# Kernel optimization log

Measured on AMD Instinct MI355X. Metric: run time of the kernel, lower is better.

Reference implementation:

```python
import jax, jax.numpy as jnp
import numpy as np

HEADS = 4
N_ROUNDS = 2
R_LSH = 1.0
PH, PW = 8, 8  # patch size


def _forward(x, Wq, Wk, Wv, Wo, alpha, beta, q_w, q_b, fmam_w, fmam_b, dw_w):
    b, c, H, W = x.shape
    nh, nw = H // PH, W // PW
    # b,c,H,W -> b,H,W,c -> (b*nh*nw, PH*PW, c) patch sequences
    xi = jnp.transpose(x, (0, 2, 3, 1))
    xp = xi.reshape(b, nh, PH, nw, PW, c).transpose(0, 1, 3, 2, 4, 5)
    xp = xp.reshape(b * nh * nw, PH * PW, c)
    B, N, _ = xp.shape

    q = xp @ Wq  # (B,N,3c)
    k = xp @ Wk
    v = xp @ Wv
    d = q.shape[-1] // HEADS

    def split_heads(t):
        # 'b t (h e) -> (b h) t e'
        return t.reshape(B, N, HEADS, -1).transpose(0, 2, 1, 3).reshape(B * HEADS, N, -1)

    qh, kh, vh = split_heads(q), split_heads(k), split_heads(v)
    xh = split_heads(xp)  # (bs, N, c/heads) used for hashing

    # XBOX+ asymmetric transform (no_grad in original)
    norms = jnp.linalg.norm(xh, axis=-1, keepdims=True)            # (bs,N,1)
    MX = jnp.max(norms, axis=-2, keepdims=True)                    # (bs,1,1)
    ext = jnp.sqrt(jnp.maximum(MX ** 2 - norms ** 2, 0.0))
    Xs = jnp.concatenate([xh, ext, jnp.zeros_like(ext)], axis=-1)  # (bs,N,e+2)

    # SALSH projections -> bucket order via argsort
    proj = (Xs @ alpha + beta) / R_LSH                             # (bs,N,R)
    pos = jax.lax.stop_gradient(jnp.argsort(jnp.transpose(proj, (2, 0, 1)), axis=-1))  # (R,bs,N)

    def gather(t):  # (bs,N,d) -> (R,bs,N,d) permuted per round
        return jnp.take_along_axis(jnp.broadcast_to(t, (N_ROUNDS,) + t.shape), pos[..., None], axis=2)

    sq, sk, sv = gather(qh), gather(kh), gather(vh)
    # block == whole 64-token patch, attention within permuted block
    inner = jnp.einsum('rbqd,rbkd->rbqk', sq, sk)                  # (R,bs,N,N)
    lse = jax.scipy.special.logsumexp(inner, axis=-1, keepdims=True)
    dots = jnp.exp(inner - lse)
    bo = jnp.einsum('rbqk,rbkd->rbqd', dots, sv)                   # (R,bs,N,d)

    rev = jnp.argsort(pos, axis=-1)                                # inverse permutation
    o = jnp.take_along_axis(bo, rev[..., None], axis=2)            # scatter back
    logits = jnp.take_along_axis(lse[..., 0], rev, axis=2)         # (R,bs,N)
    probs = jnp.exp(logits - jax.scipy.special.logsumexp(logits, axis=0, keepdims=True))
    out = jnp.sum(o * probs[..., None], axis=0)                    # (bs,N,d)

    out = out.reshape(B, HEADS, N, d).transpose(0, 2, 1, 3).reshape(B, N, HEADS * d)
    out = out @ Wo                                                 # (B,N,c)
    F_spa = out.reshape(b, nh, nw, PH, PW, c).transpose(0, 1, 3, 2, 4, 5).reshape(b, H, W, c)
    spa = jnp.transpose(F_spa, (0, 3, 1, 2))                       # (b,c,H,W)

    # FMAM stand-in: global-context module producing (b,c,c) frequency context
    xf = x.reshape(b, c, H * W)
    keys = jax.nn.softmax(jnp.einsum('oc,bcn->bon', fmam_w, xf) + fmam_b[None, :, None], axis=-1)
    ctx = jnp.einsum('bcn,bon->bco', xf, keys)                     # (b,c,c)
    queries = jax.nn.softmax(jnp.einsum('oc,bcn->bon', q_w, xf) + q_b[None, :, None], axis=1)
    freq = jnp.einsum('bck,bcn->bkn', ctx, queries).reshape(b, c, H, W)

    # depthwise Conv3d kernel (2,1,1), no bias -> per-channel weighted sum
    return spa * dw_w[:, 0][None, :, None, None] + freq * dw_w[:, 1][None, :, None, None]


def setup_inputs() -> dict:
    key = jax.random.key(0)
    ks = jax.random.split(key, 12)
    b, c, H, W = 2, 64, 256, 256
    inner = 3 * c
    e = c // HEADS
    s = 0.02
    return {
        'x': jax.random.normal(ks[0], (b, c, H, W), jnp.float32),
        'Wq': jax.random.normal(ks[1], (c, inner), jnp.float32) * s,
        'Wk': jax.random.normal(ks[2], (c, inner), jnp.float32) * s,
        'Wv': jax.random.normal(ks[3], (c, inner), jnp.float32) * s,
        'Wo': jax.random.normal(ks[4], (inner, c), jnp.float32) * s,
        'alpha': jax.random.normal(ks[5], (e + 2, N_ROUNDS), jnp.float32),
        'beta': jax.random.uniform(ks[6], (1, N_ROUNDS), jnp.float32, 0.0, R_LSH),
        'q_w': jax.random.normal(ks[7], (c, c), jnp.float32) * s,
        'q_b': jnp.zeros((c,), jnp.float32),
        'fmam_w': jax.random.normal(ks[8], (c, c), jnp.float32) * s,
        'fmam_b': jnp.zeros((c,), jnp.float32),
        'dw_w': jax.random.normal(ks[9], (c, 2), jnp.float32) * 0.5,
    }


def reference(x, Wq, Wk, Wv, Wo, alpha, beta, q_w, q_b, fmam_w, fmam_b, dw_w):
    return _forward(x, Wq, Wk, Wv, Wo, alpha, beta, q_w, q_b, fmam_w, fmam_b, dw_w)
```

## Files before the change

### kernel.cpp

```cpp
#include <hip/hip_runtime.h>
#include <hip/hip_bf16.h>


typedef __attribute__((ext_vector_type(8))) short bf16x8;
typedef __attribute__((ext_vector_type(4))) float f32x4;
typedef __attribute__((ext_vector_type(4))) unsigned u32x4;

static __device__ __forceinline__ short f2bf(float f) {
  __hip_bfloat16 h = __float2bfloat16(f);
  return *reinterpret_cast<short*>(&h);
}
static __device__ __forceinline__ float bf2f(short s) {
  return __uint_as_float(((unsigned)(unsigned short)s) << 16);
}
static __device__ __forceinline__ unsigned pack2bf(float a, float b) {
  return (unsigned)(unsigned short)f2bf(a) | ((unsigned)(unsigned short)f2bf(b) << 16);
}
static __device__ __forceinline__ f32x4 MFMA(bf16x8 a, bf16x8 b, f32x4 c) {
  return __builtin_amdgcn_mfma_f32_16x16x32_bf16(a, b, c, 0, 0, 0);
}

#define LSWZ(row, bytecol) ((((row) << 7) + (bytecol)) ^ (((row) & 7) << 4))

static __device__ __forceinline__ bf16x8 repack(
    unsigned pl0, unsigned pl1, unsigned ph0, unsigned ph1,
    int srcA, int srcB, bool hi) {
  unsigned l0 = __shfl((int)pl0, srcA, 64), l1 = __shfl((int)pl1, srcA, 64);
  unsigned l2 = __shfl((int)pl0, srcB, 64), l3 = __shfl((int)pl1, srcB, 64);
  unsigned h0 = __shfl((int)ph0, srcA, 64), h1 = __shfl((int)ph1, srcA, 64);
  unsigned h2 = __shfl((int)ph0, srcB, 64), h3 = __shfl((int)ph1, srcB, 64);
  u32x4 v;
  v[0] = hi ? h0 : l0; v[1] = hi ? h1 : l1;
  v[2] = hi ? h2 : l2; v[3] = hi ? h3 : l3;
  return __builtin_bit_cast(bf16x8, v);
}
static __device__ __forceinline__ bf16x8 repack1(
    unsigned pl0, unsigned pl1, int srcA, int srcB, bool hi) {
  unsigned l0 = __shfl((int)pl0, srcA, 64), l1 = __shfl((int)pl1, srcA, 64);
  unsigned l2 = __shfl((int)pl0, srcB, 64), l3 = __shfl((int)pl1, srcB, 64);
  u32x4 v;
  v[0] = hi ? 0u : l0; v[1] = hi ? 0u : l1;
  v[2] = hi ? 0u : l2; v[3] = hi ? 0u : l3;
  return __builtin_bit_cast(bf16x8, v);
}

static __device__ __forceinline__ bf16x8 load_xfrag(const float* xg, int c0, int n) {
  bf16x8 r;
#pragma unroll
  for (int j = 0; j < 8; ++j) r[j] = f2bf(xg[((size_t)(c0 + j) << 16) + (size_t)n]);
  return r;
}

__global__ __launch_bounds__(256) void prep_w(
    const float* __restrict__ Wq, const float* __restrict__ Wk,
    const float* __restrict__ Wv, const float* __restrict__ Wo,
    const float* __restrict__ fw, const float* __restrict__ qw,
    short* __restrict__ Wt3, short* __restrict__ Wvb,
    short* __restrict__ WoT2, short* __restrict__ fwb, short* __restrict__ qwb)
{
  int i = blockIdx.x * 256 + threadIdx.x;
  if (i < 24576) {
    int m = i / 12288, rem = i % 12288;
    int r = rem >> 6, c = rem & 63;
    const float* W = m ? Wk : Wq;
    Wt3[i] = f2bf(W[c * 192 + r]);
  }
  if (i < 12288) {
    int h = i / 3072, rem = i % 3072;
    int j = rem & 7, ln = (rem >> 3) & 63, dcks = rem >> 9;
    int dc = dcks >> 1, ks = dcks & 1;
    int c = 32 * ks + 8 * (ln >> 4) + j;
    int col = 48 * h + 16 * dc + (ln & 15);
    Wvb[i] = f2bf(Wv[c * 192 + col]);
  }
  if (i < 12288) {
    int co = i / 192, dg = i % 192;
    WoT2[i] = f2bf(Wo[dg * 64 + co]);
  }
  if (i < 4096) { fwb[i] = f2bf(fw[i]); qwb[i] = f2bf(qw[i]); }
}

__global__ __launch_bounds__(256, 3) void attn_fused(
    const float* __restrict__ x, const short* __restrict__ Wt3,
    const short* __restrict__ Wvb, const short* __restrict__ WoT2,
    const short* __restrict__ qwb, const float* __restrict__ qbias,
    const short* __restrict__ ctxb16, const float* __restrict__ dw,
    float* __restrict__ out)
{
  __shared__ __align__(16) char ob_[25600];
  char* xb_ = ob_;

  const int tid = threadIdx.x, lane = tid & 63, w = tid >> 6;
  const int l15 = lane & 15, l4 = lane >> 4;
  const int srcA = l15 + 32 * (l4 & 1), srcB = srcA + 16;
  const bool hi = (l4 & 2) != 0;

  const int pid0 = blockIdx.x;
  const int pid = (pid0 & 7) * 256 + (pid0 >> 3);
  const int b = pid >> 10, prem = pid & 1023;
  const int y0 = (prem >> 5) << 3, x0 = (prem & 31) << 3;
  const float* xg = x + ((size_t)b << 22);

#pragma unroll
  for (int k = 0; k < 2; ++k) {
    int idx = tid + (k << 8);
    int t = idx & 63, c0 = (idx >> 6) << 3;
    const size_t pos = (size_t)((y0 + (t >> 3)) * 256 + x0 + (t & 7));
    bf16x8 v;
#pragma unroll
    for (int j = 0; j < 8; ++j) v[j] = f2bf(xg[((size_t)(c0 + j) << 16) + pos]);
    *(bf16x8*)(xb_ + LSWZ(t, c0 * 2)) = v;
  }
  __syncthreads();

  const int h = w;

  unsigned qpk[3][4][2], kpk[3][4][2];
#pragma unroll
  for (int m = 0; m < 2; ++m) {
    const short* WT = Wt3 + m * 12288 + (48 * h) * 64;
    bf16x8 a[3][2];
#pragma unroll
    for (int rp = 0; rp < 3; ++rp)
#pragma unroll
      for (int ks = 0; ks < 2; ++ks)
        a[rp][ks] = *(const bf16x8*)(WT + (16 * rp + l15) * 64 + 32 * ks + 8 * l4);
    __builtin_amdgcn_s_setprio(1);
#pragma unroll
    for (int cq = 0; cq < 4; ++cq) {
      bf16x8 b0 = *(const bf16x8*)(xb_ + LSWZ(16 * cq + l15, 16 * l4));
      bf16x8 b1 = *(const bf16x8*)(xb_ + LSWZ(16 * cq + l15, 64 + 16 * l4));
#pragma unroll
      for (int rp = 0; rp < 3; ++rp) {
        f32x4 acc = (f32x4)0.f;
        acc = MFMA(a[rp][0], b0, acc);
        acc = MFMA(a[rp][1], b1, acc);
        unsigned* dst = m ? kpk[rp][cq] : qpk[rp][cq];
        dst[0] = pack2bf(acc[0], acc[1]);
        dst[1] = pack2bf(acc[2], acc[3]);
      }
    }
    __builtin_amdgcn_s_setprio(0);
  }

  unsigned ppk[4][4][2];
  {
    bf16x8 Bq[4][2];
#pragma unroll
    for (int tt = 0; tt < 4; ++tt) {
      Bq[tt][0] = repack(qpk[0][tt][0], qpk[0][tt][1], qpk[1][tt][0], qpk[1][tt][1], srcA, srcB, hi);
      Bq[tt][1] = repack1(qpk[2][tt][0], qpk[2][tt][1], srcA, srcB, hi);
    }
    f32x4 st[4][4];
#pragma unroll
    for (int ur = 0; ur < 4; ++ur) {
      bf16x8 A0 = repack(kpk[0][ur][0], kpk[0][ur][1], kpk[1][ur][0], kpk[1][ur][1], srcA, srcB, hi);
      bf16x8 A1 = repack1(kpk[2][ur][0], kpk[2][ur][1], srcA, srcB, hi);
      __builtin_amdgcn_s_setprio(1);
#pragma unroll
      for (int tt = 0; tt < 4; ++tt) {
        f32x4 acc = (f32x4)0.f;
        acc = MFMA(A0, Bq[tt][0], acc);
        acc = MFMA(A1, Bq[tt][1], acc);
        st[ur][tt] = acc;
      }
      __builtin_amdgcn_s_setprio(0);
    }
#pragma unroll
    for (int tt = 0; tt < 4; ++tt) {
      float m = st[0][tt][0];
#pragma unroll
      for (int ur = 0; ur < 4; ++ur)
#pragma unroll
        for (int r = 0; r < 4; ++r) m = fmaxf(m, st[ur][tt][r]);
      m = fmaxf(m, __shfl_xor(m, 16, 64));
      m = fmaxf(m, __shfl_xor(m, 32, 64));
      float s = 0.f;
#pragma unroll
      for (int ur = 0; ur < 4; ++ur)
#pragma unroll
        for (int r = 0; r < 4; ++r) {
          float e = __expf(st[ur][tt][r] - m);
          st[ur][tt][r] = e; s += e;
        }
      s += __shfl_xor(s, 16, 64);
      s += __shfl_xor(s, 32, 64);
      const float inv = 1.f / s;
#pragma unroll
      for (int ur = 0; ur < 4; ++ur) {
        ppk[ur][tt][0] = pack2bf(st[ur][tt][0] * inv, st[ur][tt][1] * inv);
        ppk[ur][tt][1] = pack2bf(st[ur][tt][2] * inv, st[ur][tt][3] * inv);
      }
    }
  }

  unsigned vpk[4][3][2];
  {
    const short* Wvh = Wvb + h * 3072;
    bf16x8 bv[3][2];
#pragma unroll
    for (int dc = 0; dc < 3; ++dc)
#pragma unroll
      for (int ks = 0; ks < 2; ++ks)
        bv[dc][ks] = *(const bf16x8*)(Wvh + ((dc * 2 + ks) * 64 + lane) * 8);
    __builtin_amdgcn_s_setprio(1);
#pragma unroll
    for (int ur = 0; ur < 4; ++ur) {
      bf16x8 a0 = *(const bf16x8*)(xb_ + LSWZ(16 * ur + l15, 16 * l4));
      bf16x8 a1 = *(const bf16x8*)(xb_ + LSWZ(16 * ur + l15, 64 + 16 * l4));
#pragma unroll
      for (int dc = 0; dc < 3; ++dc) {
        f32x4 acc = (f32x4)0.f;
        acc = MFMA(a0, bv[dc][0], acc);
        acc = MFMA(a1, bv[dc][1], acc);
        vpk[ur][dc][0] = pack2bf(acc[0], acc[1]);
        vpk[ur][dc][1] = pack2bf(acc[2], acc[3]);
      }
    }
    __builtin_amdgcn_s_setprio(0);
  }

  unsigned pzpk[4][2];
  {
    bf16x8 xz0 = *(const bf16x8*)(xb_ + LSWZ(16 * w + l15, 16 * l4));
    bf16x8 xz1 = *(const bf16x8*)(xb_ + LSWZ(16 * w + l15, 64 + 16 * l4));
    f32x4 zt[4];
#pragma unroll
    for (int orr = 0; orr < 4; ++orr) {
      bf16x8 a0 = *(const bf16x8*)(qwb + (16 * orr + l15) * 64 + 8 * l4);
      bf16x8 a1 = *(const bf16x8*)(qwb + (16 * orr + l15) * 64 + 32 + 8 * l4);
      f32x4 acc;
#pragma unroll
      for (int r = 0; r < 4; ++r) acc[r] = qbias[16 * orr + 4 * l4 + r];
      acc = MFMA(a0, xz0, acc);
      acc = MFMA(a1, xz1, acc);
      zt[orr] = acc;
    }
    float m = zt[0][0];
#pragma unroll
    for (int orr = 0; orr < 4; ++orr)
#pragma unroll
      for (int r = 0; r < 4; ++r) m = fmaxf(m, zt[orr][r]);
    m = fmaxf(m, __shfl_xor(m, 16, 64));
    m = fmaxf(m, __shfl_xor(m, 32, 64));
    float s = 0.f;
#pragma unroll
    for (int orr = 0; orr < 4; ++orr)
#pragma unroll
      for (int r = 0; r < 4; ++r) { float e = __expf(zt[orr][r] - m); zt[orr][r] = e; s += e; }
    s += __shfl_xor(s, 16, 64);
    s += __shfl_xor(s, 32, 64);
    const float inv = 1.f / s;
#pragma unroll
    for (int orr = 0; orr < 4; ++orr) {
      pzpk[orr][0] = pack2bf(zt[orr][0] * inv, zt[orr][1] * inv);
      pzpk[orr][1] = pack2bf(zt[orr][2] * inv, zt[orr][3] * inv);
    }
  }
  __syncthreads();

  {
    bf16x8 Bp[4][2];
#pragma unroll
    for (int tt = 0; tt < 4; ++tt) {
      Bp[tt][0] = repack(ppk[0][tt][0], ppk[0][tt][1], ppk[1][tt][0], ppk[1][tt][1], srcA, srcB, hi);
      Bp[tt][1] = repack(ppk[2][tt][0], ppk[2][tt][1], ppk[3][tt][0], ppk[3][tt][1], srcA, srcB, hi);
    }
#pragma unroll
    for (int dr = 0; dr < 3; ++dr) {
      bf16x8 A0 = repack(vpk[0][dr][0], vpk[0][dr][1], vpk[1][dr][0], vpk[1][dr][1], srcA, srcB, hi);
      bf16x8 A1 = repack(vpk[2][dr][0], vpk[2][dr][1], vpk[3][dr][0], vpk[3][dr][1], srcA, srcB, hi);
      __builtin_amdgcn_s_setprio(1);
#pragma unroll
      for (int tt = 0; tt < 4; ++tt) {
        f32x4 acc = (f32x4)0.f;
        acc = MFMA(A0, Bp[tt][0], acc);
        acc = MFMA(A1, Bp[tt][1], acc);
        const int row = 16 * tt + l15;
        const int col = 48 * h + 16 * dr + 4 * l4;
        *(unsigned*)(ob_ + row * 400 + col * 2)     = pack2bf(acc[0], acc[1]);
        *(unsigned*)(ob_ + row * 400 + col * 2 + 4) = pack2bf(acc[2], acc[3]);
      }
      __builtin_amdgcn_s_setprio(0);
    }
  }
  __syncthreads();

  {
    f32x4 ot[4], ft[4];
#pragma unroll
    for (int kr = 0; kr < 4; ++kr) { ot[kr] = (f32x4)0.f; ft[kr] = (f32x4)0.f; }
    __builtin_amdgcn_s_setprio(1);
#pragma unroll
    for (int ks = 0; ks < 6; ++ks) {
      bf16x8 bo = *(const bf16x8*)(ob_ + (16 * w + l15) * 400 + 64 * ks + 16 * l4);
#pragma unroll
      for (int kr = 0; kr < 4; ++kr) {
        bf16x8 a = *(const bf16x8*)(WoT2 + (16 * kr + l15) * 192 + 32 * ks + 8 * l4);
        ot[kr] = MFMA(a, bo, ot[kr]);
      }
    }
    {
      bf16x8 Bz0 = repack(pzpk[0][0], pzpk[0][1], pzpk[1][0], pzpk[1][1], srcA, srcB, hi);
      bf16x8 Bz1 = repack(pzpk[2][0], pzpk[2][1], pzpk[3][0], pzpk[3][1], srcA, srcB, hi);
      const short* cb = ctxb16 + ((size_t)b << 12);
#pragma unroll
      for (int kr = 0; kr < 4; ++kr) {
        bf16x8 a0 = *(const bf16x8*)(cb + (16 * kr + l15) * 64 + 8 * l4);
        bf16x8 a1 = *(const bf16x8*)(cb + (16 * kr + l15) * 64 + 32 + 8 * l4);
        ft[kr] = MFMA(a0, Bz0, ft[kr]);
        ft[kr] = MFMA(a1, Bz1, ft[kr]);
      }
    }
    __builtin_amdgcn_s_setprio(0);
    const int t = 16 * w + l15;
    const size_t nbase = (size_t)((y0 + (t >> 3)) * 256 + x0 + (t & 7));
    float* og = out + ((size_t)b << 22);
#pragma unroll
    for (int kr = 0; kr < 4; ++kr)
#pragma unroll
      for (int r = 0; r < 4; ++r) {
        const int co = 16 * kr + 4 * l4 + r;
        og[((size_t)co << 16) + nbase] = ot[kr][r] * dw[2 * co] + ft[kr][r] * dw[2 * co + 1];
      }
  }
}

__global__ __launch_bounds__(256) void fmam_ctx1(
    const float* __restrict__ x, const short* __restrict__ fwb,
    const float* __restrict__ fb, float* __restrict__ ctxpart,
    float* __restrict__ epart)
{
  __shared__ short cred16[4][64 * 68];
  __shared__ float ered[4][64];
  const int tid = threadIdx.x, lane = tid & 63, w = tid >> 6;
  const int l15 = lane & 15, l4 = lane >> 4;
  const int srcA = l15 + 32 * (l4 & 1), srcB = srcA + 16;
  const bool hi = (l4 & 2) != 0;
  const int chunk = blockIdx.x, b = blockIdx.y;
  const float* xg = x + ((size_t)b << 22);
  const int n0 = (chunk << 8) + (w << 6);

  bf16x8 Bfw[4][2];
#pragma unroll
  for (int ct = 0; ct < 4; ++ct)
#pragma unroll
    for (int ks = 0; ks < 2; ++ks)
      Bfw[ct][ks] = *(const bf16x8*)(fwb + (16 * ct + l15) * 64 + 32 * ks + 8 * l4);
  float fbl[4];
#pragma unroll
  for (int ct = 0; ct < 4; ++ct) fbl[ct] = fb[16 * ct + l15];

  f32x4 acc[4][4];
#pragma unroll
  for (int i = 0; i < 4; ++i)
#pragma unroll
    for (int j = 0; j < 4; ++j) acc[i][j] = (f32x4)0.f;
  float esum[4] = {0.f, 0.f, 0.f, 0.f};

#pragma unroll
  for (int ns = 0; ns < 2; ++ns) {
    const int nb = n0 + 32 * ns;
    bf16x8 axT[2][2];
#pragma unroll
    for (int rt = 0; rt < 2; ++rt)
#pragma unroll
      for (int ks = 0; ks < 2; ++ks)
        axT[rt][ks] = load_xfrag(xg, 32 * ks + 8 * l4, nb + 16 * rt + l15);
    unsigned pl[4][2][2];
#pragma unroll
    for (int rt = 0; rt < 2; ++rt)
#pragma unroll
      for (int ct = 0; ct < 4; ++ct) {
        f32x4 yt = (f32x4)(fbl[ct]);
        yt = MFMA(axT[rt][0], Bfw[ct][0], yt);
        yt = MFMA(axT[rt][1], Bfw[ct][1], yt);
        float e0 = __expf(yt[0]), e1 = __expf(yt[1]);
        float e2 = __expf(yt[2]), e3 = __expf(yt[3]);
        esum[ct] += (e0 + e1) + (e2 + e3);
        pl[ct][rt][0] = pack2bf(e0, e1);
        pl[ct][rt][1] = pack2bf(e2, e3);
      }
    bf16x8 axc[4];
#pragma unroll
    for (int rt2 = 0; rt2 < 4; ++rt2) {
      const float* xr = xg + ((size_t)(16 * rt2 + l15) << 16) + nb + 8 * l4;
      const float4 a4 = *(const float4*)xr;
      const float4 b4 = *(const float4*)(xr + 4);
      bf16x8 f;
      f[0] = f2bf(a4.x); f[1] = f2bf(a4.y); f[2] = f2bf(a4.z); f[3] = f2bf(a4.w);
      f[4] = f2bf(b4.x); f[5] = f2bf(b4.y); f[6] = f2bf(b4.z); f[7] = f2bf(b4.w);
      axc[rt2] = f;
    }
#pragma unroll
    for (int ct = 0; ct < 4; ++ct) {
      bf16x8 Bp = repack(pl[ct][0][0], pl[ct][0][1], pl[ct][1][0], pl[ct][1][1],
                         srcA, srcB, hi);
#pragma unroll
      for (int rt2 = 0; rt2 < 4; ++rt2)
        acc[rt2][ct] = MFMA(axc[rt2], Bp, acc[rt2][ct]);
    }
  }
#pragma unroll
  for (int ct = 0; ct < 4; ++ct) {
    esum[ct] += __shfl_xor(esum[ct], 16, 64);
    esum[ct] += __shfl_xor(esum[ct], 32, 64);
  }
  if (l4 == 0) {
#pragma unroll
    for (int ct = 0; ct < 4; ++ct) ered[w][16 * ct + l15] = esum[ct];
  }
#pragma unroll
  for (int ct = 0; ct < 4; ++ct)
#pragma unroll
    for (int rt2 = 0; rt2 < 4; ++rt2) {
      uint2 pr;
      pr.x = pack2bf(acc[rt2][ct][0], acc[rt2][ct][1]);
      pr.y = pack2bf(acc[rt2][ct][2], acc[rt2][ct][3]);
      *(uint2*)&cred16[w][(16 * ct + l15) * 68 + 16 * rt2 + 4 * l4] = pr;
    }
  __syncthreads();
  float* cp = ctxpart + ((((size_t)b << 8) + chunk) << 12);
  for (int i = tid; i < 4096; i += 256) {
    const int o = i >> 6, c = i & 63;
    const int li = o * 68 + c;
    cp[i] = (bf2f(cred16[0][li]) + bf2f(cred16[1][li])) +
            (bf2f(cred16[2][li]) + bf2f(cred16[3][li]));
  }
  if (tid < 64)
    epart[(((b << 8) + chunk) << 6) + tid] =
        (ered[0][tid] + ered[1][tid]) + (ered[2][tid] + ered[3][tid]);
}

__global__ __launch_bounds__(256) void fmam_ctxreduce2(
    const float* __restrict__ ctxpart, const float* __restrict__ epart,
    short* __restrict__ ctxb16)
{
  __shared__ float red[256];
  __shared__ float invs;
  const int bo = blockIdx.x;
  const int b = bo >> 6, o = bo & 63;
  const int tid = threadIdx.x;
  red[tid] = epart[(((b << 8) + tid) << 6) + o];
  __syncthreads();
  if (tid < 64) {
    float v = red[tid] + red[tid + 64] + red[tid + 128] + red[tid + 192];
#pragma unroll
    for (int m = 1; m <= 32; m <<= 1) v += __shfl_xor(v, m, 64);
    if (tid == 0) invs = 1.f / v;
  }
  __syncthreads();
  const float inv = invs;
  const int c = tid & 63, cg = tid >> 6;
  const float* p = ctxpart + ((size_t)b << 20) + (o << 6) + c;
  float s = 0.f;
  for (int ch = cg * 64; ch < cg * 64 + 64; ++ch) s += p[(size_t)ch << 12];
  __syncthreads();
  red[tid] = s;
  __syncthreads();
  if (tid < 64) {
    const float v = red[tid] + red[tid + 64] + red[tid + 128] + red[tid + 192];
    ctxb16[(bo << 6) + tid] = f2bf(v * inv);
  }
}

extern "C" void kernel_launch(void* const* d_in, const int* in_sizes, int n_in,
                              void* d_out, int out_size, void* d_ws, size_t ws_size,
                              hipStream_t stream) {
  const float* x  = (const float*)d_in[0];
  const float* Wq = (const float*)d_in[1];
  const float* Wk = (const float*)d_in[2];
  const float* Wv = (const float*)d_in[3];
  const float* Wo = (const float*)d_in[4];
  const float* qw = (const float*)d_in[7];
  const float* qb = (const float*)d_in[8];
  const float* fw = (const float*)d_in[9];
  const float* fb = (const float*)d_in[10];
  const float* dw = (const float*)d_in[11];
  float* out = (float*)d_out;

  float* ws = (float*)d_ws;
  float* ctxpart = ws;
  float* epart   = ctxpart + 2097152;
  short* wbuf    = (short*)(epart + 32768);
  short* Wt3  = wbuf;
  short* Wvb  = Wt3 + 24576;
  short* WoT2 = Wvb + 12288;
  short* fwb  = WoT2 + 12288;
  short* qwb  = fwb + 4096;
  short* ctxb16 = qwb + 4096;

  hipLaunchKernelGGL(prep_w, dim3(96), dim3(256), 0, stream,
                     Wq, Wk, Wv, Wo, fw, qw, Wt3, Wvb, WoT2, fwb, qwb);
  hipLaunchKernelGGL(fmam_ctx1, dim3(256, 2), dim3(256), 0, stream,
                     x, fwb, fb, ctxpart, epart);
  hipLaunchKernelGGL(fmam_ctxreduce2, dim3(128), dim3(256), 0, stream,
                     ctxpart, epart, ctxb16);
  hipLaunchKernelGGL(attn_fused, dim3(2048), dim3(256), 0, stream,
                     x, Wt3, Wvb, WoT2, qwb, qb, ctxb16, dw, out);
}
```

Before: 108.7 us.

## Drop softmax max-subtraction, defer normalization, and split fmam context pass across more blocks

Attention and query softmaxes now exponentiate raw logits with no max reduction. Normalization is deferred: the attention reciprocal is applied after the PV MFMA and the query-softmax reciprocal in the final output blend, which removes max shuffles and per-element rescaling. The fmam context kernel now runs twice as many blocks, each covering half the tokens, with partial buffers and the reduce kernel enlarged to match. Skipping max-subtraction risks overflow if logits are large, and doubling the partials adds workspace and reduction traffic.

Result: slower. 129.0 us (+18.6%).

```diff
diff --git a/kernel.cpp b/kernel.cpp
--- a/kernel.cpp
+++ b/kernel.cpp
@@ -144,6 +144,7 @@
   }
 
   unsigned ppk[4][4][2];
+  float invs[4];
   {
     bf16x8 Bq[4][2];
 #pragma unroll
@@ -151,7 +152,7 @@
       Bq[tt][0] = repack(qpk[0][tt][0], qpk[0][tt][1], qpk[1][tt][0], qpk[1][tt][1], srcA, srcB, hi);
       Bq[tt][1] = repack1(qpk[2][tt][0], qpk[2][tt][1], srcA, srcB, hi);
     }
-    f32x4 st[4][4];
+    float esum[4] = {0.f, 0.f, 0.f, 0.f};
 #pragma unroll
     for (int ur = 0; ur < 4; ++ur) {
       bf16x8 A0 = repack(kpk[0][ur][0], kpk[0][ur][1], kpk[1][ur][0], kpk[1][ur][1], srcA, srcB, hi);
@@ -162,35 +163,19 @@
         f32x4 acc = (f32x4)0.f;
         acc = MFMA(A0, Bq[tt][0], acc);
         acc = MFMA(A1, Bq[tt][1], acc);
-        st[ur][tt] = acc;
+        float e0 = __expf(acc[0]), e1 = __expf(acc[1]);
+        float e2 = __expf(acc[2]), e3 = __expf(acc[3]);
+        esum[tt] += (e0 + e1) + (e2 + e3);
+        ppk[ur][tt][0] = pack2bf(e0, e1);
+        ppk[ur][tt][1] = pack2bf(e2, e3);
       }
       __builtin_amdgcn_s_setprio(0);
     }
 #pragma unroll
     for (int tt = 0; tt < 4; ++tt) {
-      float m = st[0][tt][0];
-#pragma unroll
-      for (int ur = 0; ur < 4; ++ur)
-#pragma unroll
-        for (int r = 0; r < 4; ++r) m = fmaxf(m, st[ur][tt][r]);
-      m = fmaxf(m, __shfl_xor(m, 16, 64));
-      m = fmaxf(m, __shfl_xor(m, 32, 64));
-      float s = 0.f;
-#pragma unroll
-      for (int ur = 0; ur < 4; ++ur)
-#pragma unroll
-        for (int r = 0; r < 4; ++r) {
-          float e = __expf(st[ur][tt][r] - m);
-          st[ur][tt][r] = e; s += e;
-        }
-      s += __shfl_xor(s, 16, 64);
-      s += __shfl_xor(s, 32, 64);
-      const float inv = 1.f / s;
-#pragma unroll
-      for (int ur = 0; ur < 4; ++ur) {
-        ppk[ur][tt][0] = pack2bf(st[ur][tt][0] * inv, st[ur][tt][1] * inv);
-        ppk[ur][tt][1] = pack2bf(st[ur][tt][2] * inv, st[ur][tt][3] * inv);
-      }
+      esum[tt] += __shfl_xor(esum[tt], 16, 64);
+      esum[tt] += __shfl_xor(esum[tt], 32, 64);
+      invs[tt] = 1.f / esum[tt];
     }
   }
 
@@ -221,10 +206,11 @@
   }
 
   unsigned pzpk[4][2];
+  float invz;
   {
     bf16x8 xz0 = *(const bf16x8*)(xb_ + LSWZ(16 * w + l15, 16 * l4));
     bf16x8 xz1 = *(const bf16x8*)(xb_ + LSWZ(16 * w + l15, 64 + 16 * l4));
-    f32x4 zt[4];
+    float zs = 0.f;
 #pragma unroll
     for (int orr = 0; orr < 4; ++orr) {
       bf16x8 a0 = *(const bf16x8*)(qwb + (16 * orr + l15) * 64 + 8 * l4);
@@ -234,28 +220,15 @@
       for (int r = 0; r < 4; ++r) acc[r] = qbias[16 * orr + 4 * l4 + r];
       acc = MFMA(a0, xz0, acc);
       acc = MFMA(a1, xz1, acc);
-      zt[orr] = acc;
-    }
-    float m = zt[0][0];
-#pragma unroll
-    for (int orr = 0; orr < 4; ++orr)
-#pragma unroll
-      for (int r = 0; r < 4; ++r) m = fmaxf(m, zt[orr][r]);
-    m = fmaxf(m, __shfl_xor(m, 16, 64));
-    m = fmaxf(m, __shfl_xor(m, 32, 64));
-    float s = 0.f;
-#pragma unroll
-    for (int orr = 0; orr < 4; ++orr)
-#pragma unroll
-      for (int r = 0; r < 4; ++r) { float e = __expf(zt[orr][r] - m); zt[orr][r] = e; s += e; }
-    s += __shfl_xor(s, 16, 64);
-    s += __shfl_xor(s, 32, 64);
-    const float inv = 1.f / s;
-#pragma unroll
-    for (int orr = 0; orr < 4; ++orr) {
-      pzpk[orr][0] = pack2bf(zt[orr][0] * inv, zt[orr][1] * inv);
-      pzpk[orr][1] = pack2bf(zt[orr][2] * inv, zt[orr][3] * inv);
-    }
+      float e0 = __expf(acc[0]), e1 = __expf(acc[1]);
+      float e2 = __expf(acc[2]), e3 = __expf(acc[3]);
+      zs += (e0 + e1) + (e2 + e3);
+      pzpk[orr][0] = pack2bf(e0, e1);
+      pzpk[orr][1] = pack2bf(e2, e3);
+    }
+    zs += __shfl_xor(zs, 16, 64);
+    zs += __shfl_xor(zs, 32, 64);
+    invz = 1.f / zs;
   }
   __syncthreads();
 
@@ -276,10 +249,11 @@
         f32x4 acc = (f32x4)0.f;
         acc = MFMA(A0, Bp[tt][0], acc);
         acc = MFMA(A1, Bp[tt][1], acc);
+        const float iv = invs[tt];
         const int row = 16 * tt + l15;
         const int col = 48 * h + 16 * dr + 4 * l4;
-        *(unsigned*)(ob_ + row * 400 + col * 2)     = pack2bf(acc[0], acc[1]);
-        *(unsigned*)(ob_ + row * 400 + col * 2 + 4) = pack2bf(acc[2], acc[3]);
+        *(unsigned*)(ob_ + row * 400 + col * 2)     = pack2bf(acc[0] * iv, acc[1] * iv);
+        *(unsigned*)(ob_ + row * 400 + col * 2 + 4) = pack2bf(acc[2] * iv, acc[3] * iv);
       }
       __builtin_amdgcn_s_setprio(0);
     }
@@ -321,7 +295,8 @@
 #pragma unroll
       for (int r = 0; r < 4; ++r) {
         const int co = 16 * kr + 4 * l4 + r;
-        og[((size_t)co << 16) + nbase] = ot[kr][r] * dw[2 * co] + ft[kr][r] * dw[2 * co + 1];
+        og[((size_t)co << 16) + nbase] =
+            ot[kr][r] * dw[2 * co] + ft[kr][r] * invz * dw[2 * co + 1];
       }
   }
 }
@@ -339,7 +314,7 @@
   const bool hi = (l4 & 2) != 0;
   const int chunk = blockIdx.x, b = blockIdx.y;
   const float* xg = x + ((size_t)b << 22);
-  const int n0 = (chunk << 8) + (w << 6);
+  const int nb = (chunk << 7) + (w << 5);
 
   bf16x8 Bfw[4][2];
 #pragma unroll
@@ -358,9 +333,7 @@
     for (int j = 0; j < 4; ++j) acc[i][j] = (f32x4)0.f;
   float esum[4] = {0.f, 0.f, 0.f, 0.f};
 
-#pragma unroll
-  for (int ns = 0; ns < 2; ++ns) {
-    const int nb = n0 + 32 * ns;
+  {
     bf16x8 axT[2][2];
 #pragma unroll
     for (int rt = 0; rt < 2; ++rt)
@@ -420,7 +393,7 @@
       *(uint2*)&cred16[w][(16 * ct + l15) * 68 + 16 * rt2 + 4 * l4] = pr;
     }
   __syncthreads();
-  float* cp = ctxpart + ((((size_t)b << 8) + chunk) << 12);
+  float* cp = ctxpart + ((((size_t)b << 9) + chunk) << 12);
   for (int i = tid; i < 4096; i += 256) {
     const int o = i >> 6, c = i & 63;
     const int li = o * 68 + c;
@@ -428,7 +401,7 @@
             (bf2f(cred16[2][li]) + bf2f(cred16[3][li]));
   }
   if (tid < 64)
-    epart[(((b << 8) + chunk) << 6) + tid] =
+    epart[((((size_t)b << 9) + chunk) << 6) + tid] =
         (ered[0][tid] + ered[1][tid]) + (ered[2][tid] + ered[3][tid]);
 }
 
@@ -441,7 +414,8 @@
   const int bo = blockIdx.x;
   const int b = bo >> 6, o = bo & 63;
   const int tid = threadIdx.x;
-  red[tid] = epart[(((b << 8) + tid) << 6) + o];
+  red[tid] = epart[((((size_t)b << 9) + tid) << 6) + o] +
+             epart[((((size_t)b << 9) + tid + 256) << 6) + o];
   __syncthreads();
   if (tid < 64) {
     float v = red[tid] + red[tid + 64] + red[tid + 128] + red[tid + 192];
@@ -452,9 +426,9 @@
   __syncthreads();
   const float inv = invs;
   const int c = tid & 63, cg = tid >> 6;
-  const float* p = ctxpart + ((size_t)b << 20) + (o << 6) + c;
+  const float* p = ctxpart + ((size_t)b << 21) + (o << 6) + c;
   float s = 0.f;
-  for (int ch = cg * 64; ch < cg * 64 + 64; ++ch) s += p[(size_t)ch << 12];
+  for (int ch = cg * 128; ch < cg * 128 + 128; ++ch) s += p[(size_t)ch << 12];
   __syncthreads();
   red[tid] = s;
   __syncthreads();
@@ -481,8 +455,8 @@
 
   float* ws = (float*)d_ws;
   float* ctxpart = ws;
-  float* epart   = ctxpart + 2097152;
-  short* wbuf    = (short*)(epart + 32768);
+  float* epart   = ctxpart + 4194304;
+  short* wbuf    = (short*)(epart + 65536);
   short* Wt3  = wbuf;
   short* Wvb  = Wt3 + 24576;
   short* WoT2 = Wvb + 12288;
@@ -492,7 +466,7 @@
 
   hipLaunchKernelGGL(prep_w, dim3(96), dim3(256), 0, stream,
                      Wq, Wk, Wv, Wo, fw, qw, Wt3, Wvb, WoT2, fwb, qwb);
-  hipLaunchKernelGGL(fmam_ctx1, dim3(256, 2), dim3(256), 0, stream,
+  hipLaunchKernelGGL(fmam_ctx1, dim3(512, 2), dim3(256), 0, stream,
                      x, fwb, fb, ctxpart, epart);
   hipLaunchKernelGGL(fmam_ctxreduce2, dim3(128), dim3(256), 0, stream,
                      ctxpart, epart, ctxb16);
```
